# Performance work log

Measured on AMD Instinct MI355X. Metric: run time of the kernel, lower is better.

## Reference

```python
import jax, jax.numpy as jnp
import numpy as np

D_MODEL = 1024
NHEAD = 16
DIM_HEAD = D_MODEL // NHEAD  # 64
SCALE = DIM_HEAD ** -0.5


def _rope_freqs():
    # freqs list = 10000^(-i/32) for i in 0..31 (len == dim_head//2), then cat [f, -f]
    half = 10000.0 ** (-jnp.arange(DIM_HEAD // 2, dtype=jnp.float32) / (DIM_HEAD // 2))
    return jnp.concatenate([half, -half], axis=0)  # [dim_head]


def _rotate_half(t):
    t1, t2 = jnp.split(t, 2, axis=-1)
    return jnp.concatenate([t2, t1], axis=-1)


def setup_inputs() -> dict:
    key = jax.random.key(0)
    ks = jax.random.split(key, 6)
    B, S = 4, 2048
    x = jax.random.normal(ks[0], (B, S, D_MODEL), dtype=jnp.float32)
    p = jnp.broadcast_to(jnp.arange(S, dtype=jnp.int32), (B, S))
    lim_qkv = (1.0 / D_MODEL) ** 0.5
    Wqkv_w = jax.random.uniform(ks[1], (3 * D_MODEL, D_MODEL), jnp.float32, -lim_qkv, lim_qkv)
    Wqkv_b = jax.random.uniform(ks[2], (3 * D_MODEL,), jnp.float32, -lim_qkv, lim_qkv)
    Wo_w = jax.random.uniform(ks[3], (D_MODEL, D_MODEL), jnp.float32, -lim_qkv, lim_qkv)
    Wo_b = jax.random.uniform(ks[4], (D_MODEL,), jnp.float32, -lim_qkv, lim_qkv)
    return {"x": x, "p": p, "Wqkv_w": Wqkv_w, "Wqkv_b": Wqkv_b, "Wo_w": Wo_w, "Wo_b": Wo_b}


def reference(x, p, Wqkv_w, Wqkv_b, Wo_w, Wo_b):
    B, S, D = x.shape
    qkv = (x @ Wqkv_w.T + Wqkv_b).reshape(B, S, 3, NHEAD, DIM_HEAD)
    # torch: transpose(3,1) -> (B, H, 3, S, Dh), unbind dim=2
    q = jnp.transpose(qkv[:, :, 0], (0, 2, 1, 3))  # [B,H,S,Dh]
    k = jnp.transpose(qkv[:, :, 1], (0, 2, 1, 3))
    v = jnp.transpose(qkv[:, :, 2], (0, 2, 1, 3))
    freqs = _rope_freqs()
    ang = p[..., None].astype(jnp.float32) * freqs  # [B,S,Dh]
    cos = jnp.cos(ang)[:, None]  # [B,1,S,Dh] broadcasts over heads
    sin = jnp.sin(ang)[:, None]
    q = q * cos + _rotate_half(q) * sin
    k = k * cos + _rotate_half(k) * sin
    scores = jnp.einsum("bhqd,bhkd->bhqk", q, k) * SCALE
    attn = jax.nn.softmax(scores, axis=-1)
    out = jnp.einsum("bhqk,bhkd->bhqd", attn, v)
    out = jnp.transpose(out, (0, 2, 1, 3)).reshape(B, S, D)
    return out @ Wo_w.T + Wo_b
```

## Files before the change

### kernel.cpp

```cpp
#include <hip/hip_runtime.h>
#include <hip/hip_bf16.h>
#include <cmath>

constexpr int D_MODEL = 1024;
constexpr int NHEAD   = 16;
constexpr int DH      = 64;
constexpr int BATCH   = 4;
constexpr int SEQ     = 2048;
constexpr int TOKENS  = BATCH * SEQ;
constexpr float SCALE = 0.125f;
constexpr float QSF   = 0.125f * 1.44269504088896340736f;

typedef __attribute__((ext_vector_type(8))) short bf16x8;
typedef __attribute__((ext_vector_type(4))) short short4v;
typedef __attribute__((ext_vector_type(4))) float f32x4;
typedef __attribute__((ext_vector_type(4))) unsigned u32x4;

__device__ inline short f2bf(float f) {
    union { float f; unsigned u; } v; v.f = f;
    unsigned r = v.u + 0x7FFFu + ((v.u >> 16) & 1u);
    return (short)(r >> 16);
}
__device__ inline float bf2f(short s) {
    union { float f; unsigned u; } v;
    v.u = ((unsigned)(unsigned short)s) << 16;
    return v.f;
}
__device__ inline void llds16(const void* g, void* l) {
    __builtin_amdgcn_global_load_lds(
        (const __attribute__((address_space(1))) unsigned*)g,
        (__attribute__((address_space(3))) unsigned*)l, 16, 0, 0);
}

constexpr int N8_X    = TOKENS * 1024 / 8;
constexpr int N8_WQKV = 3072 * 1024 / 8;
constexpr int N8_WO   = 1024 * 1024 / 8;

__global__ __launch_bounds__(256) void cvt3_bf16_kernel(
    const float* __restrict__ sx, const float* __restrict__ sq,
    const float* __restrict__ so,
    short* __restrict__ dx, short* __restrict__ dq, short* __restrict__ dw)
{
    int i = blockIdx.x * blockDim.x + threadIdx.x;
    const float* src; short* dst; int off;
    if (i < N8_X)                  { src = sx; dst = dx;  off = i; }
    else if (i < N8_X + N8_WQKV)   { src = sq; dst = dq;  off = i - N8_X; }
    else                           { src = so; dst = dw;  off = i - N8_X - N8_WQKV; }
    const float4* s = (const float4*)src + (size_t)off * 2;
    float4 a = s[0], b = s[1];
    bf16x8 v;
    v[0] = f2bf(a.x); v[1] = f2bf(a.y); v[2] = f2bf(a.z); v[3] = f2bf(a.w);
    v[4] = f2bf(b.x); v[5] = f2bf(b.y); v[6] = f2bf(b.z); v[7] = f2bf(b.w);
    *(bf16x8*)(dst + (size_t)off * 8) = v;
}

template<int OUT_BF16, int ROPE>
__global__ __launch_bounds__(256) void gemm_mfma_kernel(
    const short* __restrict__ A, const short* __restrict__ B,
    const float* __restrict__ bias, void* __restrict__ C,
    const int* __restrict__ p, int M, int N, int K)
{
    __shared__ short As[128 * 64];
    __shared__ short Bs[128 * 64];
    const int tid  = threadIdx.x;
    const int w    = tid >> 6;
    const int lane = tid & 63;
    const int q16  = lane & 15;
    const int quad = lane >> 4;
    const int wm   = (w & 1) * 64;
    const int wn   = (w >> 1) * 64;
    const int bm   = blockIdx.x * 128;
    const int bn   = blockIdx.y * 128;

    const int srow = w * 32 + (lane >> 3);
    const int kcs  = lane & 7;

    f32x4 acc[4][4];
    #pragma unroll
    for (int i = 0; i < 4; i++)
        #pragma unroll
        for (int j = 0; j < 4; j++) acc[i][j] = (f32x4){0.f, 0.f, 0.f, 0.f};

    for (int k0 = 0; k0 < K; k0 += 64) {
        __syncthreads();
        #pragma unroll
        for (int i = 0; i < 4; i++) {
            int row = srow + i * 8;
            int kc  = kcs ^ (row & 7);
            const short* ga = A + (size_t)(bm + row) * K + k0 + kc * 8;
            const short* gb = B + (size_t)(bn + row) * K + k0 + kc * 8;
            short* la = &As[(w * 32 + i * 8) * 64];
            short* lb = &Bs[(w * 32 + i * 8) * 64];
            llds16(ga, la);
            llds16(gb, lb);
        }
        __syncthreads();
        #pragma unroll
        for (int ks = 0; ks < 2; ks++) {
            bf16x8 af[4], bfr[4];
            #pragma unroll
            for (int t = 0; t < 4; t++) {
                int ra = wm + t * 16 + q16;
                int ca = (ks * 4 + quad) ^ (ra & 7);
                af[t]  = *(const bf16x8*)&As[ra * 64 + ca * 8];
                int rb = wn + t * 16 + q16;
                int cb = (ks * 4 + quad) ^ (rb & 7);
                bfr[t] = *(const bf16x8*)&Bs[rb * 64 + cb * 8];
            }
            #pragma unroll
            for (int mb = 0; mb < 4; mb++)
                #pragma unroll
                for (int nb = 0; nb < 4; nb++)
                    acc[mb][nb] = __builtin_amdgcn_mfma_f32_16x16x32_bf16(
                        af[mb], bfr[nb], acc[mb][nb], 0, 0, 0);
        }
    }

    if (ROPE && (bn + wn) < 2 * D_MODEL) {
        const float sf = (bn + wn) < D_MODEL ? QSF : 1.0f;
        float posv[4][4];
        #pragma unroll
        for (int mb = 0; mb < 4; mb++) {
            const int rm = bm + wm + mb * 16 + quad * 4;
            #pragma unroll
            for (int r = 0; r < 4; r++) posv[mb][r] = (float)p[rm + r];
        }
        #pragma unroll
        for (int nb = 0; nb < 2; nb++) {
            const int i   = nb * 16 + q16;
            const int cn0 = bn + wn + i;
            const int cn1 = cn0 + 32;
            const float b0 = bias[cn0], b1 = bias[cn1];
            const float fr = __builtin_amdgcn_exp2f((float)i * -0.4152410118609203f)
                             * 0.15915494309189535f;
            #pragma unroll
            for (int mb = 0; mb < 4; mb++) {
                const int rm = bm + wm + mb * 16 + quad * 4;
                #pragma unroll
                for (int r = 0; r < 4; r++) {
                    float t = posv[mb][r] * fr;
                    t -= floorf(t);
                    float sn = __builtin_amdgcn_sinf(t);
                    float c  = __builtin_amdgcn_cosf(t);
                    float v0 = acc[mb][nb][r]     + b0;
                    float v1 = acc[mb][nb + 2][r] + b1;
                    ((short*)C)[(size_t)(rm + r) * N + cn0] =
                        f2bf(fmaf(v0, c,  v1 * sn) * sf);
                    ((short*)C)[(size_t)(rm + r) * N + cn1] =
                        f2bf(fmaf(v1, c, -v0 * sn) * sf);
                }
            }
        }
        return;
    }

    #pragma unroll
    for (int nb = 0; nb < 4; nb++) {
        const int cn = bn + wn + nb * 16 + q16;
        const float bv = bias[cn];
        #pragma unroll
        for (int mb = 0; mb < 4; mb++) {
            const int rm = bm + wm + mb * 16 + quad * 4;
            #pragma unroll
            for (int r = 0; r < 4; r++) {
                float v = acc[mb][nb][r] + bv;
                if (OUT_BF16)
                    ((short*)C)[(size_t)(rm + r) * N + cn] = f2bf(v);
                else
                    ((float*)C)[(size_t)(rm + r) * N + cn] = v;
            }
        }
    }
}

__global__ __launch_bounds__(256, 2) void attn_mfma_kernel(
    const short* __restrict__ qkv, short* __restrict__ out)
{
    __shared__ short Ks[2][64 * 64];
    __shared__ short Vs[2][64 * 64];

    const int tid  = threadIdx.x;
    const int w    = tid >> 6;
    const int lane = tid & 63;
    const int q16  = lane & 15;
    const int quad = lane >> 4;
    const int gid  = blockIdx.x;
    const int bh   = gid & 63;
    const int qblk = gid >> 6;
    const int b    = bh >> 4;
    const int h    = bh & 15;
    const int qtok0 = qblk * 256 + w * 64;

    bf16x8 qf[4][2];
    #pragma unroll
    for (int qb = 0; qb < 4; qb++) {
        const short* Qrow =
            qkv + (size_t)(b * SEQ + qtok0 + qb * 16 + q16) * 3072 + h * 64;
        qf[qb][0] = *(const bf16x8*)(Qrow + quad * 8);
        qf[qb][1] = *(const bf16x8*)(Qrow + 32 + quad * 8);
    }

    f32x4 o[4][4];
    #pragma unroll
    for (int qb = 0; qb < 4; qb++)
        #pragma unroll
        for (int md = 0; md < 4; md++) o[qb][md] = (f32x4){0.f, 0.f, 0.f, 0.f};
    float lsum[4] = {0.f, 0.f, 0.f, 0.f};

    const short* Kg = qkv + (size_t)b * SEQ * 3072 + 1024 + h * 64;
    const short* Vg = Kg + 1024;

    const int krow = w * 16 + (lane >> 3);
    const int kc   = (lane & 7) ^ (krow & 7);
    const int vkey = (tid & 31) * 2;
    const int vdb  = (tid >> 5) * 8;
    const int vL   = ((vkey >> 5) << 2) | (((vkey >> 3) & 1) << 1) | ((vkey >> 4) & 1);

    auto vwrite = [&](int buf, const uint4& a, const uint4& bb) {
        #pragma unroll
        for (int j = 0; j < 8; j++) {
            unsigned lo = (j & 1) ? 0x07060302u : 0x05040100u;
            unsigned sa = (&a.x)[j >> 1], sb = (&bb.x)[j >> 1];
            *(unsigned*)&Vs[buf][(vdb + j) * 64 + ((vL ^ j) << 3) + (vkey & 7)] =
                __builtin_amdgcn_perm(sb, sa, lo);
        }
    };

    {
        llds16(Kg + (size_t)krow * 3072 + kc * 8, &Ks[0][(w * 16) * 64]);
        llds16(Kg + (size_t)(krow + 8) * 3072 + kc * 8, &Ks[0][(w * 16 + 8) * 64]);
        const short* vsrc = Vg + (size_t)vkey * 3072 + vdb;
        uint4 a  = *(const uint4*)vsrc;
        uint4 bb = *(const uint4*)(vsrc + 3072);
        vwrite(0, a, bb);
    }
    __syncthreads();

    int cur = 0;
    for (int t = 0; t < SEQ / 64; t++) {
        uint4 pva, pvb;
        const bool pf = (t < SEQ / 64 - 1);
        if (pf) {
            const int ktn = (t + 1) * 64;
            llds16(Kg + (size_t)(ktn + krow) * 3072 + kc * 8,
                   &Ks[cur ^ 1][(w * 16) * 64]);
            llds16(Kg + (size_t)(ktn + krow + 8) * 3072 + kc * 8,
                   &Ks[cur ^ 1][(w * 16 + 8) * 64]);
            const short* vsrc = Vg + (size_t)(ktn + vkey) * 3072 + vdb;
            pva = *(const uint4*)vsrc;
            pvb = *(const uint4*)(vsrc + 3072);
        }

        bf16x8 af[4][2], av[4][2];
        #pragma unroll
        for (int mb = 0; mb < 4; mb++) {
            #pragma unroll
            for (int ks = 0; ks < 2; ks++) {
                int c = (((ks * 4 + quad) ^ (q16 & 7))) * 8;
                af[mb][ks] = *(const bf16x8*)&Ks[cur][(mb * 16 + q16) * 64 + c];
                av[mb][ks] = *(const bf16x8*)&Vs[cur][(mb * 16 + q16) * 64 + c];
            }
        }

        #pragma unroll
        for (int qb = 0; qb < 4; qb++) {
            f32x4 sc[4];
            #pragma unroll
            for (int mb = 0; mb < 4; mb++) {
                f32x4 c = {0.f, 0.f, 0.f, 0.f};
                c = __builtin_amdgcn_mfma_f32_16x16x32_bf16(af[mb][0], qf[qb][0], c, 0, 0, 0);
                c = __builtin_amdgcn_mfma_f32_16x16x32_bf16(af[mb][1], qf[qb][1], c, 0, 0, 0);
                sc[mb] = c;
            }
            float ltile = 0.f;
            unsigned da[4], db[4];
            #pragma unroll
            for (int mb = 0; mb < 2; mb++) {
                float p0 = __builtin_amdgcn_exp2f(sc[mb][0]);
                float p1 = __builtin_amdgcn_exp2f(sc[mb][1]);
                float p2 = __builtin_amdgcn_exp2f(sc[mb][2]);
                float p3 = __builtin_amdgcn_exp2f(sc[mb][3]);
                ltile += (p0 + p1) + (p2 + p3);
                asm("v_cvt_pk_bf16_f32 %0, %1, %2" : "=v"(da[mb]) : "v"(p0), "v"(p1));
                asm("v_cvt_pk_bf16_f32 %0, %1, %2" : "=v"(db[mb]) : "v"(p2), "v"(p3));
            }
            asm("v_permlane16_swap_b32 %0, %1" : "+v"(da[0]), "+v"(da[1]));
            asm("v_permlane16_swap_b32 %0, %1" : "+v"(db[0]), "+v"(db[1]));
            union { u32x4 u; bf16x8 v; } pb0;
            pb0.u = (u32x4){da[0], db[0], da[1], db[1]};
            #pragma unroll
            for (int mb = 2; mb < 4; mb++) {
                float p0 = __builtin_amdgcn_exp2f(sc[mb][0]);
                float p1 = __builtin_amdgcn_exp2f(sc[mb][1]);
                float p2 = __builtin_amdgcn_exp2f(sc[mb][2]);
                float p3 = __builtin_amdgcn_exp2f(sc[mb][3]);
                ltile += (p0 + p1) + (p2 + p3);
                asm("v_cvt_pk_bf16_f32 %0, %1, %2" : "=v"(da[mb]) : "v"(p0), "v"(p1));
                asm("v_cvt_pk_bf16_f32 %0, %1, %2" : "=v"(db[mb]) : "v"(p2), "v"(p3));
            }
            #pragma unroll
            for (int md = 0; md < 4; md++)
                o[qb][md] = __builtin_amdgcn_mfma_f32_16x16x32_bf16(
                    av[md][0], pb0.v, o[qb][md], 0, 0, 0);
            asm("v_permlane16_swap_b32 %0, %1" : "+v"(da[2]), "+v"(da[3]));
            asm("v_permlane16_swap_b32 %0, %1" : "+v"(db[2]), "+v"(db[3]));
            union { u32x4 u; bf16x8 v; } pb1;
            pb1.u = (u32x4){da[2], db[2], da[3], db[3]};
            #pragma unroll
            for (int md = 0; md < 4; md++)
                o[qb][md] = __builtin_amdgcn_mfma_f32_16x16x32_bf16(
                    av[md][1], pb1.v, o[qb][md], 0, 0, 0);
            lsum[qb] += ltile;
        }

        if (pf) vwrite(cur ^ 1, pva, pvb);
        __syncthreads();
        cur ^= 1;
    }

    #pragma unroll
    for (int qb = 0; qb < 4; qb++) {
        float l = lsum[qb];
        l += __shfl_xor(l, 16);
        l += __shfl_xor(l, 32);
        float inv = 1.f / l;
        short* orow = out + (size_t)(b * SEQ + qtok0 + qb * 16 + q16) * 1024
                      + h * 64 + quad * 4;
        #pragma unroll
        for (int md = 0; md < 4; md++) {
            short4v t;
            t[0] = f2bf(o[qb][md][0] * inv);
            t[1] = f2bf(o[qb][md][1] * inv);
            t[2] = f2bf(o[qb][md][2] * inv);
            t[3] = f2bf(o[qb][md][3] * inv);
            *(short4v*)(orow + md * 16) = t;
        }
    }
}

extern "C" void kernel_launch(void* const* d_in, const int* in_sizes, int n_in,
                              void* d_out, int out_size, void* d_ws, size_t ws_size,
                              hipStream_t stream)
{
    (void)in_sizes; (void)n_in; (void)out_size; (void)ws_size;
    const float* x      = (const float*)d_in[0];
    const int*   p      = (const int*)  d_in[1];
    const float* Wqkv_w = (const float*)d_in[2];
    const float* Wqkv_b = (const float*)d_in[3];
    const float* Wo_w   = (const float*)d_in[4];
    const float* Wo_b   = (const float*)d_in[5];
    float* out = (float*)d_out;

    short* xb     = (short*)d_ws;
    short* wqkvb  = xb + (size_t)TOKENS * 1024;
    short* wob    = wqkvb + (size_t)3072 * 1024;
    short* qkvb   = wob + (size_t)1024 * 1024;
    short* attnob = qkvb + (size_t)TOKENS * 3072;

    dim3 blk(256);

    cvt3_bf16_kernel<<<dim3((N8_X + N8_WQKV + N8_WO) / 256), blk, 0, stream>>>(
        x, Wqkv_w, Wo_w, xb, wqkvb, wob);

    gemm_mfma_kernel<1, 1><<<dim3(TOKENS / 128, 3072 / 128), blk, 0, stream>>>(
        xb, wqkvb, Wqkv_b, qkvb, p, TOKENS, 3072, 1024);

    attn_mfma_kernel<<<dim3(512), blk, 0, stream>>>(qkvb, attnob);

    gemm_mfma_kernel<0, 0><<<dim3(TOKENS / 128, 1024 / 128), blk, 0, stream>>>(
        attnob, wob, Wo_b, out, nullptr, TOKENS, 1024, 1024);
}
```

Before: 261.5 us.

## Add double-buffered 256x128 eight-wave GEMM for QKV projection with RoPE

Replaces the QKV projection GEMM with a new 512-thread kernel that uses 256x128 tiles and double-buffered LDS filled by direct global-to-LDS loads. The next K tile is prefetched while MFMAs run on the current one, with explicit waitcnt/barrier and setprio scheduling. This targets the load-then-compute serialisation of the old single-buffer kernel. It needs 96KB of dynamic shared memory, which limits occupancy, and relies on hand-written synchronisation that could race if the vmcnt counts are wrong. The output-projection GEMM is simplified to an fp32-only version with no speed change intended.

After: 262.3 us. About the same (+0.3%).

```diff
diff --git a/kernel.cpp b/kernel.cpp
--- a/kernel.cpp
+++ b/kernel.cpp
@@ -54,11 +54,163 @@
     *(bf16x8*)(dst + (size_t)off * 8) = v;
 }
 
-template<int OUT_BF16, int ROPE>
+template<int ROPE>
+__global__ __launch_bounds__(512, 2) void gemm8p_mfma_kernel(
+    const short* __restrict__ A, const short* __restrict__ B,
+    const float* __restrict__ bias, short* __restrict__ C,
+    const int* __restrict__ p, int M, int N, int K)
+{
+    extern __shared__ short smem[];
+    short* Asm = smem;
+    short* Bsm = smem + 2 * 256 * 64;
+
+    const int tid  = threadIdx.x;
+    const int w    = tid >> 6;
+    const int lane = tid & 63;
+    const int q16  = lane & 15;
+    const int quad = lane >> 4;
+    const int wm   = (w >> 1) * 64;
+    const int wn   = (w & 1) * 64;
+    const int bm   = blockIdx.x * 256;
+    const int bn   = blockIdx.y * 128;
+    const int NT   = K >> 6;
+
+    const int rowbase = tid >> 3;
+    const int ch      = tid & 7;
+    const int chs     = ch ^ (rowbase & 7);
+
+    auto stage = [&](int buf, int tt) {
+        const int k0 = tt * 64;
+        #pragma unroll
+        for (int i = 0; i < 4; i++) {
+            int r = i * 64 + rowbase;
+            llds16(A + (size_t)(bm + r) * K + k0 + chs * 8,
+                   &Asm[buf * (256 * 64) + r * 64 + ch * 8]);
+        }
+        #pragma unroll
+        for (int i = 0; i < 2; i++) {
+            int r = i * 64 + rowbase;
+            llds16(B + (size_t)(bn + r) * K + k0 + chs * 8,
+                   &Bsm[buf * (128 * 64) + r * 64 + ch * 8]);
+        }
+    };
+
+    f32x4 acc[4][4];
+    #pragma unroll
+    for (int i = 0; i < 4; i++)
+        #pragma unroll
+        for (int j = 0; j < 4; j++) acc[i][j] = (f32x4){0.f, 0.f, 0.f, 0.f};
+
+    stage(0, 0);
+    stage(1, 1);
+    asm volatile("s_waitcnt vmcnt(6)" ::: "memory");
+    asm volatile("s_barrier" ::: "memory");
+
+    const int swA = quad ^ (q16 & 7);
+    for (int t = 0; t < NT; t++) {
+        const int c = t & 1;
+        const short* as = &Asm[c * (256 * 64)];
+        const short* bs = &Bsm[c * (128 * 64)];
+
+        {
+            bf16x8 af0[4], bf0[4];
+            #pragma unroll
+            for (int i = 0; i < 4; i++) {
+                af0[i] = *(const bf16x8*)&as[(wm + i * 16 + q16) * 64 + swA * 8];
+                bf0[i] = *(const bf16x8*)&bs[(wn + i * 16 + q16) * 64 + swA * 8];
+            }
+            asm volatile("s_barrier" ::: "memory");
+            __builtin_amdgcn_s_setprio(1);
+            #pragma unroll
+            for (int mb = 0; mb < 4; mb++)
+                #pragma unroll
+                for (int nb = 0; nb < 4; nb++)
+                    acc[mb][nb] = __builtin_amdgcn_mfma_f32_16x16x32_bf16(
+                        af0[mb], bf0[nb], acc[mb][nb], 0, 0, 0);
+            __builtin_amdgcn_s_setprio(0);
+            asm volatile("s_barrier" ::: "memory");
+        }
+        {
+            bf16x8 af1[4], bf1[4];
+            const int swB = (4 + quad) ^ (q16 & 7);
+            #pragma unroll
+            for (int i = 0; i < 4; i++) {
+                af1[i] = *(const bf16x8*)&as[(wm + i * 16 + q16) * 64 + swB * 8];
+                bf1[i] = *(const bf16x8*)&bs[(wn + i * 16 + q16) * 64 + swB * 8];
+            }
+            asm volatile("s_waitcnt lgkmcnt(0)" ::: "memory");
+            __builtin_amdgcn_sched_barrier(0);
+            asm volatile("s_barrier" ::: "memory");
+            const bool pf2 = (t + 2 < NT);
+            if (pf2) stage(c, t + 2);
+            __builtin_amdgcn_s_setprio(1);
+            #pragma unroll
+            for (int mb = 0; mb < 4; mb++)
+                #pragma unroll
+                for (int nb = 0; nb < 4; nb++)
+                    acc[mb][nb] = __builtin_amdgcn_mfma_f32_16x16x32_bf16(
+                        af1[mb], bf1[nb], acc[mb][nb], 0, 0, 0);
+            __builtin_amdgcn_s_setprio(0);
+            if (pf2) asm volatile("s_waitcnt vmcnt(6)" ::: "memory");
+            else     asm volatile("s_waitcnt vmcnt(0)" ::: "memory");
+            asm volatile("s_barrier" ::: "memory");
+        }
+    }
+
+    if (ROPE && (bn + wn) < 2 * D_MODEL) {
+        const float sf = (bn + wn) < D_MODEL ? QSF : 1.0f;
+        float posv[4][4];
+        #pragma unroll
+        for (int mb = 0; mb < 4; mb++) {
+            const int rm = bm + wm + mb * 16 + quad * 4;
+            #pragma unroll
+            for (int r = 0; r < 4; r++) posv[mb][r] = (float)p[rm + r];
+        }
+        #pragma unroll
+        for (int nb = 0; nb < 2; nb++) {
+            const int i   = nb * 16 + q16;
+            const int cn0 = bn + wn + i;
+            const int cn1 = cn0 + 32;
+            const float b0 = bias[cn0], b1 = bias[cn1];
+            const float fr = __builtin_amdgcn_exp2f((float)i * -0.4152410118609203f)
+                             * 0.15915494309189535f;
+            #pragma unroll
+            for (int mb = 0; mb < 4; mb++) {
+                const int rm = bm + wm + mb * 16 + quad * 4;
+                #pragma unroll
+                for (int r = 0; r < 4; r++) {
+                    float t = posv[mb][r] * fr;
+                    t -= floorf(t);
+                    float sn = __builtin_amdgcn_sinf(t);
+                    float c  = __builtin_amdgcn_cosf(t);
+                    float v0 = acc[mb][nb][r]     + b0;
+                    float v1 = acc[mb][nb + 2][r] + b1;
+                    C[(size_t)(rm + r) * N + cn0] = f2bf(fmaf(v0, c,  v1 * sn) * sf);
+                    C[(size_t)(rm + r) * N + cn1] = f2bf(fmaf(v1, c, -v0 * sn) * sf);
+                }
+            }
+        }
+        return;
+    }
+
+    #pragma unroll
+    for (int nb = 0; nb < 4; nb++) {
+        const int cn = bn + wn + nb * 16 + q16;
+        const float bv = bias[cn];
+        #pragma unroll
+        for (int mb = 0; mb < 4; mb++) {
+            const int rm = bm + wm + mb * 16 + quad * 4;
+            #pragma unroll
+            for (int r = 0; r < 4; r++)
+                C[(size_t)(rm + r) * N + cn] = f2bf(acc[mb][nb][r] + bv);
+        }
+    }
+}
+
 __global__ __launch_bounds__(256) void gemm_mfma_kernel(
     const short* __restrict__ A, const short* __restrict__ B,
-    const float* __restrict__ bias, void* __restrict__ C,
-    const int* __restrict__ p, int M, int N, int K)
+    const float* __restrict__ bias, float* __restrict__ C,
+    int M, int N, int K)
 {
     __shared__ short As[128 * 64];
     __shared__ short Bs[128 * 64];
@@ -89,10 +241,8 @@
             int kc  = kcs ^ (row & 7);
             const short* ga = A + (size_t)(bm + row) * K + k0 + kc * 8;
             const short* gb = B + (size_t)(bn + row) * K + k0 + kc * 8;
-            short* la = &As[(w * 32 + i * 8) * 64];
-            short* lb = &Bs[(w * 32 + i * 8) * 64];
-            llds16(ga, la);
-            llds16(gb, lb);
+            llds16(ga, &As[(w * 32 + i * 8) * 64]);
+            llds16(gb, &Bs[(w * 32 + i * 8) * 64]);
         }
         __syncthreads();
         #pragma unroll
@@ -116,44 +266,6 @@
         }
     }
 
-    if (ROPE && (bn + wn) < 2 * D_MODEL) {
-        const float sf = (bn + wn) < D_MODEL ? QSF : 1.0f;
-        float posv[4][4];
-        #pragma unroll
-        for (int mb = 0; mb < 4; mb++) {
-            const int rm = bm + wm + mb * 16 + quad * 4;
-            #pragma unroll
-            for (int r = 0; r < 4; r++) posv[mb][r] = (float)p[rm + r];
-        }
-        #pragma unroll
-        for (int nb = 0; nb < 2; nb++) {
-            const int i   = nb * 16 + q16;
-            const int cn0 = bn + wn + i;
-            const int cn1 = cn0 + 32;
-            const float b0 = bias[cn0], b1 = bias[cn1];
-            const float fr = __builtin_amdgcn_exp2f((float)i * -0.4152410118609203f)
-                             * 0.15915494309189535f;
-            #pragma unroll
-            for (int mb = 0; mb < 4; mb++) {
-                const int rm = bm + wm + mb * 16 + quad * 4;
-                #pragma unroll
-                for (int r = 0; r < 4; r++) {
-                    float t = posv[mb][r] * fr;
-                    t -= floorf(t);
-                    float sn = __builtin_amdgcn_sinf(t);
-                    float c  = __builtin_amdgcn_cosf(t);
-                    float v0 = acc[mb][nb][r]     + b0;
-                    float v1 = acc[mb][nb + 2][r] + b1;
-                    ((short*)C)[(size_t)(rm + r) * N + cn0] =
-                        f2bf(fmaf(v0, c,  v1 * sn) * sf);
-                    ((short*)C)[(size_t)(rm + r) * N + cn1] =
-                        f2bf(fmaf(v1, c, -v0 * sn) * sf);
-                }
-            }
-        }
-        return;
-    }
-
     #pragma unroll
     for (int nb = 0; nb < 4; nb++) {
         const int cn = bn + wn + nb * 16 + q16;
@@ -162,13 +274,8 @@
         for (int mb = 0; mb < 4; mb++) {
             const int rm = bm + wm + mb * 16 + quad * 4;
             #pragma unroll
-            for (int r = 0; r < 4; r++) {
-                float v = acc[mb][nb][r] + bv;
-                if (OUT_BF16)
-                    ((short*)C)[(size_t)(rm + r) * N + cn] = f2bf(v);
-                else
-                    ((float*)C)[(size_t)(rm + r) * N + cn] = v;
-            }
+            for (int r = 0; r < 4; r++)
+                C[(size_t)(rm + r) * N + cn] = acc[mb][nb][r] + bv;
         }
     }
 }
@@ -362,11 +469,17 @@
     cvt3_bf16_kernel<<<dim3((N8_X + N8_WQKV + N8_WO) / 256), blk, 0, stream>>>(
         x, Wqkv_w, Wo_w, xb, wqkvb, wob);
 
-    gemm_mfma_kernel<1, 1><<<dim3(TOKENS / 128, 3072 / 128), blk, 0, stream>>>(
+    static bool attr_done = false;
+    if (!attr_done) {
+        hipFuncSetAttribute(reinterpret_cast<const void*>(&gemm8p_mfma_kernel<1>),
+                            hipFuncAttributeMaxDynamicSharedMemorySize, 98304);
+        attr_done = true;
+    }
+    gemm8p_mfma_kernel<1><<<dim3(TOKENS / 256, 3072 / 128), dim3(512), 98304, stream>>>(
         xb, wqkvb, Wqkv_b, qkvb, p, TOKENS, 3072, 1024);
 
     attn_mfma_kernel<<<dim3(512), blk, 0, stream>>>(qkvb, attnob);
 
-    gemm_mfma_kernel<0, 0><<<dim3(TOKENS / 128, 1024 / 128), blk, 0, stream>>>(
-        attnob, wob, Wo_b, out, nullptr, TOKENS, 1024, 1024);
-}
+    gemm_mfma_kernel<<<dim3(TOKENS / 128, 1024 / 128), blk, 0, stream>>>(
+        attnob, wob, Wo_b, out, TOKENS, 1024, 1024);
+}
```

## Rewrite GEMMs as 256x128 tiles with triple-buffered LDS pipeline and XCD-aware mapping

Applied to the files above, without the earlier changes.

Replaces the 128x128 single-buffered GEMM with a 512-thread, 256x128 tile kernel that triple-buffers LDS through dynamic shared memory. Global-to-LDS loads for the next tiles are issued ahead and tracked with explicit vmcnt waits, so memory latency overlaps the MFMA work, and setprio raises wave priority during the MFMA block. Blocks are remapped so each XCD works on contiguous M tiles, which should improve L2 reuse. The cost is much more LDS per block (about 144KB) and hand-written waitcnt and barrier logic that must match the number of loads issued per stage.

Result: no change. 262.4 us (+0.3%).

```diff
diff --git a/kernel.cpp b/kernel.cpp
--- a/kernel.cpp
+++ b/kernel.cpp
@@ -54,26 +54,53 @@
     *(bf16x8*)(dst + (size_t)off * 8) = v;
 }
 
-template<int OUT_BF16, int ROPE>
-__global__ __launch_bounds__(256) void gemm_mfma_kernel(
+template<int ROPE, int OUTBF>
+__global__ __launch_bounds__(512, 2) void gemm8p_mfma_kernel(
     const short* __restrict__ A, const short* __restrict__ B,
     const float* __restrict__ bias, void* __restrict__ C,
     const int* __restrict__ p, int M, int N, int K)
 {
-    __shared__ short As[128 * 64];
-    __shared__ short Bs[128 * 64];
+    extern __shared__ short smem[];
+    constexpr int BUFSZ = (256 + 128) * 64;
+
     const int tid  = threadIdx.x;
     const int w    = tid >> 6;
     const int lane = tid & 63;
     const int q16  = lane & 15;
     const int quad = lane >> 4;
-    const int wm   = (w & 1) * 64;
-    const int wn   = (w >> 1) * 64;
-    const int bm   = blockIdx.x * 128;
-    const int bn   = blockIdx.y * 128;
-
-    const int srow = w * 32 + (lane >> 3);
-    const int kcs  = lane & 7;
+    const int wm   = (w >> 1) * 64;
+    const int wn   = (w & 1) * 64;
+    const int NT   = K >> 6;
+
+    const int GX  = M >> 8;
+    const int cpx = GX >> 3;
+    const int wg  = blockIdx.x;
+    const int xcd = wg & 7;
+    const int r_  = wg >> 3;
+    const int bm  = (xcd * cpx + (r_ % cpx)) * 256;
+    const int bn  = (r_ / cpx) * 128;
+
+    const int rowbase = tid >> 3;
+    const int ch      = tid & 7;
+    const int chs     = ch ^ (rowbase & 7);
+
+    auto stage = [&](int buf, int tt) {
+        const int k0 = tt * 64;
+        short* base  = smem + buf * BUFSZ;
+        #pragma unroll
+        for (int i = 0; i < 4; i++) {
+            int r = i * 64 + rowbase;
+            llds16(A + (size_t)(bm + r) * K + k0 + chs * 8,
+                   base + r * 64 + ch * 8);
+        }
+        short* bbase = base + 256 * 64;
+        #pragma unroll
+        for (int i = 0; i < 2; i++) {
+            int r = i * 64 + rowbase;
+            llds16(B + (size_t)(bn + r) * K + k0 + chs * 8,
+                   bbase + r * 64 + ch * 8);
+        }
+    };
 
     f32x4 acc[4][4];
     #pragma unroll
@@ -81,39 +108,53 @@
         #pragma unroll
         for (int j = 0; j < 4; j++) acc[i][j] = (f32x4){0.f, 0.f, 0.f, 0.f};
 
-    for (int k0 = 0; k0 < K; k0 += 64) {
-        __syncthreads();
-        #pragma unroll
-        for (int i = 0; i < 4; i++) {
-            int row = srow + i * 8;
-            int kc  = kcs ^ (row & 7);
-            const short* ga = A + (size_t)(bm + row) * K + k0 + kc * 8;
-            const short* gb = B + (size_t)(bn + row) * K + k0 + kc * 8;
-            short* la = &As[(w * 32 + i * 8) * 64];
-            short* lb = &Bs[(w * 32 + i * 8) * 64];
-            llds16(ga, la);
-            llds16(gb, lb);
-        }
-        __syncthreads();
+    stage(0, 0);
+    stage(1, 1);
+    stage(2, 2);
+    asm volatile("s_waitcnt vmcnt(12)" ::: "memory");
+    asm volatile("s_barrier" ::: "memory");
+
+    int c = 0;
+    for (int t = 0; t < NT; t++) {
+        const short* as = smem + c * BUFSZ;
+        const short* bs = as + 256 * 64;
+
+        bf16x8 af[2][4], bfr[2][4];
         #pragma unroll
         for (int ks = 0; ks < 2; ks++) {
-            bf16x8 af[4], bfr[4];
-            #pragma unroll
-            for (int t = 0; t < 4; t++) {
-                int ra = wm + t * 16 + q16;
-                int ca = (ks * 4 + quad) ^ (ra & 7);
-                af[t]  = *(const bf16x8*)&As[ra * 64 + ca * 8];
-                int rb = wn + t * 16 + q16;
-                int cb = (ks * 4 + quad) ^ (rb & 7);
-                bfr[t] = *(const bf16x8*)&Bs[rb * 64 + cb * 8];
-            }
+            const int sw = (ks * 4 + quad) ^ (q16 & 7);
+            #pragma unroll
+            for (int i = 0; i < 4; i++) {
+                af[ks][i]  = *(const bf16x8*)&as[(wm + i * 16 + q16) * 64 + sw * 8];
+                bfr[ks][i] = *(const bf16x8*)&bs[(wn + i * 16 + q16) * 64 + sw * 8];
+            }
+        }
+        __builtin_amdgcn_s_setprio(1);
+        #pragma unroll
+        for (int ks = 0; ks < 2; ks++)
             #pragma unroll
             for (int mb = 0; mb < 4; mb++)
                 #pragma unroll
                 for (int nb = 0; nb < 4; nb++)
                     acc[mb][nb] = __builtin_amdgcn_mfma_f32_16x16x32_bf16(
-                        af[mb], bfr[nb], acc[mb][nb], 0, 0, 0);
-        }
+                        af[ks][mb], bfr[ks][nb], acc[mb][nb], 0, 0, 0);
+        __builtin_amdgcn_s_setprio(0);
+
+        if (t + 1 < NT) {
+            asm volatile("s_waitcnt lgkmcnt(0)" ::: "memory");
+            __builtin_amdgcn_sched_barrier(0);
+            asm volatile("s_barrier" ::: "memory");
+            if (t + 3 < NT) {
+                stage(c, t + 3);
+                asm volatile("s_waitcnt vmcnt(12)" ::: "memory");
+            } else if (t + 2 < NT) {
+                asm volatile("s_waitcnt vmcnt(6)" ::: "memory");
+            } else {
+                asm volatile("s_waitcnt vmcnt(0)" ::: "memory");
+            }
+            asm volatile("s_barrier" ::: "memory");
+        }
+        c = (c == 2) ? 0 : c + 1;
     }
 
     if (ROPE && (bn + wn) < 2 * D_MODEL) {
@@ -141,13 +182,13 @@
                     float t = posv[mb][r] * fr;
                     t -= floorf(t);
                     float sn = __builtin_amdgcn_sinf(t);
-                    float c  = __builtin_amdgcn_cosf(t);
+                    float c2 = __builtin_amdgcn_cosf(t);
                     float v0 = acc[mb][nb][r]     + b0;
                     float v1 = acc[mb][nb + 2][r] + b1;
                     ((short*)C)[(size_t)(rm + r) * N + cn0] =
-                        f2bf(fmaf(v0, c,  v1 * sn) * sf);
+                        f2bf(fmaf(v0, c2,  v1 * sn) * sf);
                     ((short*)C)[(size_t)(rm + r) * N + cn1] =
-                        f2bf(fmaf(v1, c, -v0 * sn) * sf);
+                        f2bf(fmaf(v1, c2, -v0 * sn) * sf);
                 }
             }
         }
@@ -164,7 +205,7 @@
             #pragma unroll
             for (int r = 0; r < 4; r++) {
                 float v = acc[mb][nb][r] + bv;
-                if (OUT_BF16)
+                if (OUTBF)
                     ((short*)C)[(size_t)(rm + r) * N + cn] = f2bf(v);
                 else
                     ((float*)C)[(size_t)(rm + r) * N + cn] = v;
@@ -358,15 +399,27 @@
     short* attnob = qkvb + (size_t)TOKENS * 3072;
 
     dim3 blk(256);
+    constexpr int GEMM_LDS = 3 * (256 + 128) * 64 * 2;
 
     cvt3_bf16_kernel<<<dim3((N8_X + N8_WQKV + N8_WO) / 256), blk, 0, stream>>>(
         x, Wqkv_w, Wo_w, xb, wqkvb, wob);
 
-    gemm_mfma_kernel<1, 1><<<dim3(TOKENS / 128, 3072 / 128), blk, 0, stream>>>(
+    static bool attr_done = false;
+    if (!attr_done) {
+        hipFuncSetAttribute(reinterpret_cast<const void*>(&gemm8p_mfma_kernel<1, 1>),
+                            hipFuncAttributeMaxDynamicSharedMemorySize, GEMM_LDS);
+        hipFuncSetAttribute(reinterpret_cast<const void*>(&gemm8p_mfma_kernel<0, 0>),
+                            hipFuncAttributeMaxDynamicSharedMemorySize, GEMM_LDS);
+        attr_done = true;
+    }
+
+    gemm8p_mfma_kernel<1, 1><<<dim3((TOKENS / 256) * (3072 / 128)), dim3(512),
+                               GEMM_LDS, stream>>>(
         xb, wqkvb, Wqkv_b, qkvb, p, TOKENS, 3072, 1024);
 
     attn_mfma_kernel<<<dim3(512), blk, 0, stream>>>(qkvb, attnob);
 
-    gemm_mfma_kernel<0, 0><<<dim3(TOKENS / 128, 1024 / 128), blk, 0, stream>>>(
+    gemm8p_mfma_kernel<0, 0><<<dim3((TOKENS / 256) * (1024 / 128)), dim3(512),
+                               GEMM_LDS, stream>>>(
         attnob, wob, Wo_b, out, nullptr, TOKENS, 1024, 1024);
 }
```
